# Kernel optimization log

Measured on AMD Instinct MI355X. Metric: run time of the kernel, lower is better.

## Reference

```python
import jax, jax.numpy as jnp
import numpy as np

DIM = 1024
NUM_HEADS = 16
HEAD_DIM = DIM // NUM_HEADS
SCALE = HEAD_DIM ** -0.5


def apply_rope(x):
    # x: [B, H, S, D]; rotate pairs (x1, x2) split as first/second half of D
    S, D = x.shape[-2], x.shape[-1]
    pos = jnp.arange(S, dtype=jnp.float32)[:, None]                      # [S, 1]
    freqs = jnp.exp(jnp.arange(0, D, 2, dtype=jnp.float32) * (-np.log(10000.0) / D))  # [D/2]
    emb = pos * freqs                                                    # [S, D/2]
    cos = jnp.cos(emb)[None, None, :, :].astype(x.dtype)                 # [1,1,S,D/2]
    sin = jnp.sin(emb)[None, None, :, :].astype(x.dtype)
    x1, x2 = jnp.split(x, 2, axis=-1)
    return jnp.concatenate([x1 * cos - x2 * sin, x1 * sin + x2 * cos], axis=-1)


def setup_inputs() -> dict:
    key = jax.random.key(0)
    ks = jax.random.split(key, 6)
    B, S = 2, 2048
    x = jax.random.normal(ks[0], (B, S, DIM), dtype=jnp.float32)
    # torch nn.Linear weights: [out_features, in_features]
    w_std = DIM ** -0.5
    wq = jax.random.normal(ks[1], (DIM, DIM), dtype=jnp.float32) * w_std
    wk = jax.random.normal(ks[2], (DIM, DIM), dtype=jnp.float32) * w_std
    wv = jax.random.normal(ks[3], (DIM, DIM), dtype=jnp.float32) * w_std
    wo = jax.random.normal(ks[4], (DIM, DIM), dtype=jnp.float32) * w_std
    wo_b = jax.random.normal(ks[5], (DIM,), dtype=jnp.float32) * 0.01
    return {"x": x, "wq": wq, "wk": wk, "wv": wv, "wo": wo, "wo_b": wo_b}


def reference(x, wq, wk, wv, wo, wo_b):
    B, S, _ = x.shape
    def proj(w):
        # y = x @ w.T -> [B, S, dim] -> [B, H, S, head_dim]
        y = jnp.einsum('bsd,ed->bse', x, w)
        return y.reshape(B, S, NUM_HEADS, HEAD_DIM).transpose(0, 2, 1, 3)
    q = apply_rope(proj(wq))
    k = apply_rope(proj(wk))
    v = proj(wv)
    attn = jnp.einsum('bhqd,bhkd->bhqk', q, k) * SCALE   # [B,H,S,S]
    attn = jax.nn.softmax(attn, axis=-1)                 # dropout is identity in eval
    out = jnp.einsum('bhqk,bhkd->bhqd', attn, v)         # [B,H,S,D]
    out = out.transpose(0, 2, 1, 3).reshape(B, S, DIM)
    return jnp.einsum('bsd,ed->bse', out, wo) + wo_b
```

## Files before the change

### kernel.cpp

```cpp
#include <hip/hip_runtime.h>
#include <hip/hip_bf16.h>

typedef __attribute__((ext_vector_type(8))) short s16x8;
typedef __attribute__((ext_vector_type(4))) short s16x4;
typedef __attribute__((ext_vector_type(4))) float f32x4;

#define SEQ 2048
#define NB 2
#define NH 16
#define HD 64
#define DIM 1024
#define MR (NB * SEQ)
#define NT (SEQ / 64)
#define QSC 0.18033688011112042f

__device__ __forceinline__ unsigned short f2b(float f) {
    unsigned u = __float_as_uint(f);
    u += 0x7fffu + ((u >> 16) & 1u);
    return (unsigned short)(u >> 16);
}

__device__ __forceinline__ unsigned pk2(float a, float b) {
    unsigned r;
    asm("v_cvt_pk_bf16_f32 %0, %1, %2" : "=v"(r) : "v"(a), "v"(b));
    return r;
}

__device__ __forceinline__ s16x8 mk8(unsigned a, unsigned b, unsigned c, unsigned d) {
    union { unsigned u[4]; s16x8 v; } x;
    x.u[0] = a; x.u[1] = b; x.u[2] = c; x.u[3] = d;
    return x.v;
}

__device__ __forceinline__ s16x8 cat8(s16x4 a, s16x4 b) {
    union { s16x4 h[2]; s16x8 v; } x;
    x.h[0] = a; x.h[1] = b;
    return x.v;
}

__device__ __forceinline__ void gl_lds16(const unsigned short* g, unsigned short* l) {
    __builtin_amdgcn_global_load_lds(
        (const __attribute__((address_space(1))) void*)g,
        (__attribute__((address_space(3))) void*)l, 16, 0, 0);
}

__device__ __forceinline__ unsigned ldsoff(const void* p) {
    return (unsigned)(size_t)(const __attribute__((address_space(3))) void*)p;
}

__device__ __forceinline__ void cast4(const float* __restrict__ src, unsigned short* __restrict__ dst, int i) {
    float4 v = reinterpret_cast<const float4*>(src)[i];
    ushort4 o;
    o.x = f2b(v.x); o.y = f2b(v.y); o.z = f2b(v.z); o.w = f2b(v.w);
    reinterpret_cast<ushort4*>(dst)[i] = o;
}

__global__ __launch_bounds__(256) void prep_kernel(
    const float* __restrict__ x, const float* __restrict__ wq, const float* __restrict__ wk,
    const float* __restrict__ wv, const float* __restrict__ wo,
    unsigned short* __restrict__ xb, unsigned short* __restrict__ wqkv,
    unsigned short* __restrict__ wwo, float2* __restrict__ tab)
{
    int b = blockIdx.x, t = threadIdx.x;
    if (b < 4096)       cast4(x,  xb,                 b * 256 + t);
    else if (b < 5120)  cast4(wq, wqkv,               (b - 4096) * 256 + t);
    else if (b < 6144)  cast4(wk, wqkv + DIM * DIM,   (b - 5120) * 256 + t);
    else if (b < 7168)  cast4(wv, wqkv + 2 * DIM * DIM, (b - 6144) * 256 + t);
    else if (b < 8192)  cast4(wo, wwo,                (b - 7168) * 256 + t);
    else {
        int i = (b - 8192) * 256 + t;
        int pos = i >> 5, fi = i & 31;
        float freq = expf((float)fi * (-9.210340371976184f / 32.0f));
        float emb = (float)pos * freq;
        tab[i] = make_float2(cosf(emb), sinf(emb));
    }
}

template <int EPI>
__global__ __launch_bounds__(256) void gemm_mw(
    const unsigned short* __restrict__ A,
    const unsigned short* __restrict__ Bw,
    const float2* __restrict__ tab,
    unsigned short* __restrict__ qw,
    unsigned short* __restrict__ kw,
    unsigned short* __restrict__ vw,
    float* __restrict__ out,
    const float* __restrict__ bias)
{
    __shared__ unsigned short As[2][4096];
    __shared__ unsigned short Bs[2][4096];
    const int t = threadIdx.x;
    const int wid = t >> 6, lane = t & 63;
    const int wr = wid >> 1, wc = wid & 1;
    const int lo = lane & 15, hi = lane >> 4;
    const int wg = blockIdx.x;
    const int xcd = wg & 7, bi = wg >> 3;
    const int by = xcd * 4 + (bi & 3);
    const int bx = bi >> 2;
    const int m0 = by * 128, n0 = bx * 128;

    const unsigned short* agp = A + (long)(m0 + (t >> 2)) * DIM + (t & 3) * 8;
    const unsigned short* bgp = Bw + (long)(n0 + (t >> 2)) * DIM + (t & 3) * 8;
    unsigned short* alds = &As[0][0] + wid * 512;
    unsigned short* blds = &Bs[0][0] + wid * 512;

#define STG(buf, k0) {                                        \
        gl_lds16(agp + (k0), alds + (buf) * 4096);            \
        gl_lds16(agp + (k0) + 64 * DIM, alds + (buf) * 4096 + 2048); \
        gl_lds16(bgp + (k0), blds + (buf) * 4096);            \
        gl_lds16(bgp + (k0) + 64 * DIM, blds + (buf) * 4096 + 2048); }

    f32x4 acc[4][4] = {};
    STG(0, 0)
    STG(1, 32)

    for (int kt = 0; kt < 32; ++kt) {
        const int cb = kt & 1;
        if (kt < 31) { asm volatile("s_waitcnt vmcnt(4)" ::: "memory"); }
        else         { asm volatile("s_waitcnt vmcnt(0)" ::: "memory"); }
        __builtin_amdgcn_sched_barrier(0);
        __builtin_amdgcn_s_barrier();
        __builtin_amdgcn_sched_barrier(0);
        s16x8 af[4], bf[4];
#pragma unroll
        for (int i = 0; i < 4; ++i)
            af[i] = *reinterpret_cast<const s16x8*>(&As[cb][(wr * 64 + i * 16 + lo) * 32 + hi * 8]);
#pragma unroll
        for (int j = 0; j < 4; ++j)
            bf[j] = *reinterpret_cast<const s16x8*>(&Bs[cb][(wc * 64 + j * 16 + lo) * 32 + hi * 8]);
        asm volatile("s_waitcnt lgkmcnt(0)" ::: "memory");
        __builtin_amdgcn_sched_barrier(0);
        if (kt + 2 < 32) {
            __builtin_amdgcn_s_barrier();
            __builtin_amdgcn_sched_barrier(0);
            STG(cb, (kt + 2) * 32)
        }
        __builtin_amdgcn_s_setprio(1);
#pragma unroll
        for (int i = 0; i < 4; ++i)
#pragma unroll
            for (int j = 0; j < 4; ++j)
                acc[i][j] = __builtin_amdgcn_mfma_f32_16x16x32_bf16(af[i], bf[j], acc[i][j], 0, 0, 0);
        __builtin_amdgcn_s_setprio(0);
    }
#undef STG

    const int rowb = m0 + wr * 64;
    const int colb = n0 + wc * 64;
    if (EPI == 0) {
#pragma unroll
        for (int ai = 0; ai < 4; ++ai) {
#pragma unroll
            for (int cp = 0; cp < 2; ++cp) {
                f32x4 v1 = acc[ai][cp];
                f32x4 v2 = acc[ai][cp + 2];
                int e = colb + cp * 16 + lo;
                int which = e >> 10;
                int eh = e & 1023;
                int h = eh >> 6, d = eh & 63;
                unsigned short* dst = (which == 0) ? qw : ((which == 1) ? kw : vw);
                float qs = (which == 0) ? QSC : 1.0f;
#pragma unroll
                for (int r = 0; r < 4; ++r) {
                    int m = rowb + ai * 16 + hi * 4 + r;
                    int b = m >> 11, pos = m & (SEQ - 1);
                    long off = (((long)(b * NH + h)) * SEQ + pos) * HD;
                    if (which == 2) {
                        dst[off + d]      = f2b(v1[r]);
                        dst[off + d + 32] = f2b(v2[r]);
                    } else {
                        float2 cs = tab[pos * 32 + d];
                        dst[off + d]      = f2b((v1[r] * cs.x - v2[r] * cs.y) * qs);
                        dst[off + d + 32] = f2b((v1[r] * cs.y + v2[r] * cs.x) * qs);
                    }
                }
            }
        }
    } else {
#pragma unroll
        for (int ai = 0; ai < 4; ++ai)
#pragma unroll
            for (int cj = 0; cj < 4; ++cj) {
                int n = colb + cj * 16 + lo;
                float bv = bias[n];
#pragma unroll
                for (int r = 0; r < 4; ++r) {
                    int m = rowb + ai * 16 + hi * 4 + r;
                    out[(long)m * DIM + n] = acc[ai][cj][r] + bv;
                }
            }
    }
}

template <int EPI>
__global__ __launch_bounds__(64, 2) void gemm_async(
    const unsigned short* __restrict__ A,
    const unsigned short* __restrict__ Bw,
    const float2* __restrict__ tab,
    unsigned short* __restrict__ qw,
    unsigned short* __restrict__ kw,
    unsigned short* __restrict__ vw,
    float* __restrict__ out,
    const float* __restrict__ bias)
{
    __shared__ unsigned short As[2 * 2048];
    __shared__ unsigned short Bs[2 * 4096];
    const int lane = threadIdx.x & 63;
    const int lo = lane & 15, hi = lane >> 4;
    const int wg = blockIdx.x;
    const int xcd = wg & 7, bi = wg >> 3;
    const int bx = bi >> 3;
    const int by = xcd * 8 + (bi & 7);
    const int m0 = by * 64, n0 = bx * 128;

    const unsigned short* agp = A + (long)(m0 + (lane >> 2)) * DIM + (lane & 3) * 8;
    const unsigned short* bgp = Bw + (long)(n0 + (lane >> 2)) * DIM + (lane & 3) * 8;

    f32x4 acc[4][8] = {};

#define STG(buf, k0) {                                       \
        unsigned short* al = &As[(buf) * 2048];              \
        unsigned short* bl = &Bs[(buf) * 4096];              \
        _Pragma("unroll") for (int s = 0; s < 4; ++s)        \
            gl_lds16(agp + (k0) + (long)s * 16 * DIM, al + s * 512); \
        _Pragma("unroll") for (int s = 0; s < 8; ++s)        \
            gl_lds16(bgp + (k0) + (long)s * 16 * DIM, bl + s * 512); }

    STG(0, 0)
    STG(1, 32)

    for (int kt = 0; kt < 32; ++kt) {
        const int cb = kt & 1;
        if (kt < 31) { asm volatile("s_waitcnt vmcnt(12)" ::: "memory"); }
        else         { asm volatile("s_waitcnt vmcnt(0)" ::: "memory"); }
        __builtin_amdgcn_sched_barrier(0);
        s16x8 af[4], bf[8];
#pragma unroll
        for (int i = 0; i < 4; ++i)
            af[i] = *reinterpret_cast<const s16x8*>(&As[cb * 2048 + (i * 16 + lo) * 32 + hi * 8]);
#pragma unroll
        for (int j = 0; j < 8; ++j)
            bf[j] = *reinterpret_cast<const s16x8*>(&Bs[cb * 4096 + (j * 16 + lo) * 32 + hi * 8]);
        asm volatile("s_waitcnt lgkmcnt(0)" ::: "memory");
        __builtin_amdgcn_sched_barrier(0);
        if (kt + 2 < 32) STG(cb, (kt + 2) * 32)
        __builtin_amdgcn_sched_barrier(0);
        __builtin_amdgcn_s_setprio(1);
#pragma unroll
        for (int i = 0; i < 4; ++i)
#pragma unroll
            for (int j = 0; j < 8; ++j)
                acc[i][j] = __builtin_amdgcn_mfma_f32_16x16x32_bf16(af[i], bf[j], acc[i][j], 0, 0, 0);
        __builtin_amdgcn_s_setprio(0);
    }
#undef STG

    if (EPI == 0) {
    } else {
#pragma unroll
        for (int ai = 0; ai < 4; ++ai)
#pragma unroll
            for (int bj = 0; bj < 8; ++bj) {
                int n = n0 + bj * 16 + lo;
                float bv = bias[n];
#pragma unroll
                for (int r = 0; r < 4; ++r) {
                    int m = m0 + ai * 16 + hi * 4 + r;
                    out[(long)m * DIM + n] = acc[ai][bj][r] + bv;
                }
            }
    }
}

__global__ __launch_bounds__(256) void flash_attn(
    const unsigned short* __restrict__ qw,
    const unsigned short* __restrict__ kw,
    const unsigned short* __restrict__ vw,
    unsigned short* __restrict__ ao)
{
    __shared__ __align__(16) unsigned char smem[66560];
    const int t = threadIdx.x;
    const int w = t >> 6, lane = t & 63;
    const int lo = lane & 15, hi = lane >> 4;
    const int wg = blockIdx.x;
    const int swz = (wg & 7) * 128 + (wg >> 3);
    const int bh = swz >> 5;
    const int q0 = (swz & 31) * 64;
    const unsigned short* qh = qw + (long)bh * SEQ * HD;
    const unsigned short* kh = kw + (long)bh * SEQ * HD;
    const unsigned short* vh = vw + (long)bh * SEQ * HD;

    s16x8 qf[4][2];
#pragma unroll
    for (int qt = 0; qt < 4; ++qt)
#pragma unroll
        for (int ds = 0; ds < 2; ++ds)
            qf[qt][ds] = *reinterpret_cast<const s16x8*>(
                qh + (long)(q0 + qt * 16 + lo) * HD + ds * 32 + hi * 8);
    asm volatile("s_waitcnt vmcnt(0)" ::: "memory");

    unsigned char* wbase = smem + w * 16384;
    const int kr0 = lane >> 3, ks0 = (lane & 7) ^ (kr0 & 7);
    const int kr1 = 8 + (lane >> 3), ks1 = (lane & 7) ^ (kr1 & 7);
    const unsigned short* ksrc0 = kh + (16 * w + kr0) * HD + ks0 * 8;
    const unsigned short* ksrc1 = kh + (16 * w + kr1) * HD + ks1 * 8;
    const int c0 = lane, c1 = 64 + lane;
    const int kl0 = ((c0 >> 3 >> 2) << 2) | ((c0 >> 1) & 3);
    const int dd0 = (((c0 >> 3) & 3) << 4) | ((c0 & 1) << 3);
    const int kl1 = ((c1 >> 3 >> 2) << 2) | ((c1 >> 1) & 3);
    const int dd1 = (((c1 >> 3) & 3) << 4) | ((c1 & 1) << 3);
    const unsigned short* vsrc0 = vh + (16 * w + kl0) * HD + dd0;
    const unsigned short* vsrc1 = vh + (16 * w + kl1) * HD + dd1;

#define STAGE(buf, kb) {                                              \
        unsigned short* d_ = (unsigned short*)(wbase + (buf) * 4096); \
        gl_lds16(ksrc0 + (kb) * HD, d_);                              \
        gl_lds16(ksrc1 + (kb) * HD, d_ + 512);                        \
        gl_lds16(vsrc0 + (kb) * HD, d_ + 1024);                       \
        gl_lds16(vsrc1 + (kb) * HD, d_ + 1536); }

    const int kro0 = lo * 128 + ((hi ^ (lo & 7)) << 4);
    const int kro1 = lo * 128 + (((4 + hi) ^ (lo & 7)) << 4);
    const unsigned vtb0 = ldsoff(wbase) + 2048 + hi * 512 + lo * 8;

    f32x4 od[4][4] = {};
    f32x4 lr = {0.f, 0.f, 0.f, 0.f};

    STAGE(0, 0)
    STAGE(1, 64)
    STAGE(2, 128)
    STAGE(3, 192)

    constexpr int NT2 = NT / 2;
    for (int i2 = 0; i2 < NT2; ++i2) {
        const int b0 = (2 * i2) & 3;
        if (i2 < NT2 - 1) { asm volatile("s_waitcnt vmcnt(8)" ::: "memory"); }
        else              { asm volatile("s_waitcnt vmcnt(0)" ::: "memory"); }
        __builtin_amdgcn_sched_barrier(0);

        const unsigned char* bp0 = wbase + b0 * 4096;
        const unsigned char* bp1 = bp0 + 4096;
        s16x8 kf0 = *reinterpret_cast<const s16x8*>(bp0 + kro0);
        s16x8 kf1 = *reinterpret_cast<const s16x8*>(bp0 + kro1);
        s16x8 kg0 = *reinterpret_cast<const s16x8*>(bp1 + kro0);
        s16x8 kg1 = *reinterpret_cast<const s16x8*>(bp1 + kro1);
        const unsigned vta = vtb0 + b0 * 4096;
        const unsigned vtb = vta + 4096;
        s16x4 va0, va1, va2, va3, vb0, vb1, vb2, vb3;
        asm volatile("ds_read_b64_tr_b16 %0, %1"            : "=v"(va0) : "v"(vta));
        asm volatile("ds_read_b64_tr_b16 %0, %1 offset:128" : "=v"(va1) : "v"(vta));
        asm volatile("ds_read_b64_tr_b16 %0, %1 offset:256" : "=v"(va2) : "v"(vta));
        asm volatile("ds_read_b64_tr_b16 %0, %1 offset:384" : "=v"(va3) : "v"(vta));
        asm volatile("ds_read_b64_tr_b16 %0, %1"            : "=v"(vb0) : "v"(vtb));
        asm volatile("ds_read_b64_tr_b16 %0, %1 offset:128" : "=v"(vb1) : "v"(vtb));
        asm volatile("ds_read_b64_tr_b16 %0, %1 offset:256" : "=v"(vb2) : "v"(vtb));
        asm volatile("ds_read_b64_tr_b16 %0, %1 offset:384" : "=v"(vb3) : "v"(vtb));
        asm volatile("s_waitcnt lgkmcnt(0)" ::: "memory");
        __builtin_amdgcn_sched_barrier(0);

        if (i2 < NT2 - 2) {
            STAGE(b0, (2 * i2 + 4) * 64)
            STAGE(b0 + 1, (2 * i2 + 5) * 64)
        }
        __builtin_amdgcn_sched_barrier(0);

        f32x4 sc[4] = {}, sd[4] = {};
        __builtin_amdgcn_s_setprio(1);
#pragma unroll
        for (int qt = 0; qt < 4; ++qt) {
            sc[qt] = __builtin_amdgcn_mfma_f32_16x16x32_bf16(kf0, qf[qt][0], sc[qt], 0, 0, 0);
            sd[qt] = __builtin_amdgcn_mfma_f32_16x16x32_bf16(kg0, qf[qt][0], sd[qt], 0, 0, 0);
        }
#pragma unroll
        for (int qt = 0; qt < 4; ++qt) {
            sc[qt] = __builtin_amdgcn_mfma_f32_16x16x32_bf16(kf1, qf[qt][1], sc[qt], 0, 0, 0);
            sd[qt] = __builtin_amdgcn_mfma_f32_16x16x32_bf16(kg1, qf[qt][1], sd[qt], 0, 0, 0);
        }
        __builtin_amdgcn_s_setprio(0);

        s16x8 pf8[4];
#pragma unroll
        for (int qt = 0; qt < 4; ++qt) {
            float a0 = exp2f(sc[qt][0]), a1 = exp2f(sc[qt][1]);
            float a2 = exp2f(sc[qt][2]), a3 = exp2f(sc[qt][3]);
            float b0e = exp2f(sd[qt][0]), b1e = exp2f(sd[qt][1]);
            float b2e = exp2f(sd[qt][2]), b3e = exp2f(sd[qt][3]);
            lr[qt] += ((a0 + a1) + (a2 + a3)) + ((b0e + b1e) + (b2e + b3e));
            pf8[qt] = mk8(pk2(a0, a1), pk2(a2, a3), pk2(b0e, b1e), pk2(b2e, b3e));
        }
        s16x8 vf80 = cat8(va0, vb0), vf81 = cat8(va1, vb1);
        s16x8 vf82 = cat8(va2, vb2), vf83 = cat8(va3, vb3);

        __builtin_amdgcn_s_setprio(1);
#pragma unroll
        for (int qt = 0; qt < 4; ++qt) {
            od[0][qt] = __builtin_amdgcn_mfma_f32_16x16x32_bf16(vf80, pf8[qt], od[0][qt], 0, 0, 0);
            od[1][qt] = __builtin_amdgcn_mfma_f32_16x16x32_bf16(vf81, pf8[qt], od[1][qt], 0, 0, 0);
            od[2][qt] = __builtin_amdgcn_mfma_f32_16x16x32_bf16(vf82, pf8[qt], od[2][qt], 0, 0, 0);
            od[3][qt] = __builtin_amdgcn_mfma_f32_16x16x32_bf16(vf83, pf8[qt], od[3][qt], 0, 0, 0);
        }
        __builtin_amdgcn_s_setprio(0);
    }
#undef STAGE

#pragma unroll
    for (int qt = 0; qt < 4; ++qt) {
        lr[qt] += __shfl_xor(lr[qt], 16);
        lr[qt] += __shfl_xor(lr[qt], 32);
    }
    float* red = reinterpret_cast<float*>(smem);
    float* ldl = reinterpret_cast<float*>(smem + 65536);
    if (lane < 16) {
#pragma unroll
        for (int qt = 0; qt < 4; ++qt) ldl[w * 64 + qt * 16 + lane] = lr[qt];
    }

    const int b = bh >> 4, h = bh & 15;
    const int ql = w * 16 + (lane >> 2);
    const int qc = ql & 7;
    float linv = 0.f;
#pragma unroll
    for (int p = 0; p < 2; ++p) {
        __syncthreads();
#pragma unroll
        for (int dtp = 0; dtp < 2; ++dtp) {
#pragma unroll
            for (int qt = 0; qt < 4; ++qt) {
                int q = qt * 16 + lo;
                int quad = ((dtp << 2) + hi) ^ (lo & 7);
                *reinterpret_cast<f32x4*>(red + w * 4096 + q * 32 + quad * 4) = od[p * 2 + dtp][qt];
            }
        }
        __syncthreads();
        float s0[8] = {0.f, 0.f, 0.f, 0.f, 0.f, 0.f, 0.f, 0.f};
#pragma unroll
        for (int w2 = 0; w2 < 4; ++w2)
#pragma unroll
            for (int k = 0; k < 2; ++k) {
                int quad = (((lane & 3) << 1) + k) ^ qc;
                f32x4 v = *reinterpret_cast<const f32x4*>(red + w2 * 4096 + ql * 32 + quad * 4);
#pragma unroll
                for (int j = 0; j < 4; ++j) s0[k * 4 + j] += v[j];
            }
        if (p == 0)
            linv = 1.f / (ldl[ql] + ldl[64 + ql] + ldl[128 + ql] + ldl[192 + ql]);
        unsigned uu[4];
#pragma unroll
        for (int k2 = 0; k2 < 4; ++k2)
            uu[k2] = pk2(s0[2 * k2] * linv, s0[2 * k2 + 1] * linv);
        int4 ov;
        ov.x = uu[0]; ov.y = uu[1]; ov.z = uu[2]; ov.w = uu[3];
        *reinterpret_cast<int4*>(ao + ((long)(b * SEQ + q0 + ql)) * DIM +
                                 h * 64 + p * 32 + (lane & 3) * 8) = ov;
    }
}

extern "C" void kernel_launch(void* const* d_in, const int* in_sizes, int n_in,
                              void* d_out, int out_size, void* d_ws, size_t ws_size,
                              hipStream_t stream) {
    const float* x   = (const float*)d_in[0];
    const float* wq  = (const float*)d_in[1];
    const float* wk  = (const float*)d_in[2];
    const float* wv  = (const float*)d_in[3];
    const float* wo  = (const float*)d_in[4];
    const float* wob = (const float*)d_in[5];

    char* ws = (char*)d_ws;
    unsigned short* xb   = (unsigned short*)(ws);
    unsigned short* wqkv = (unsigned short*)(ws + 8388608);
    unsigned short* wwo  = (unsigned short*)(ws + 14680064);
    unsigned short* qw   = (unsigned short*)(ws + 16777216);
    unsigned short* kw   = (unsigned short*)(ws + 25165824);
    unsigned short* vw   = (unsigned short*)(ws + 33554432);
    unsigned short* ao   = (unsigned short*)(ws + 41943040);
    float2* tab          = (float2*)(ws + 50331648);

    prep_kernel<<<8448, 256, 0, stream>>>(x, wq, wk, wv, wo, xb, wqkv, wwo, tab);

    gemm_mw<0><<<768, 256, 0, stream>>>(xb, wqkv, tab, qw, kw, vw, nullptr, nullptr);
    flash_attn<<<1024, 256, 0, stream>>>(qw, kw, vw, ao);
    gemm_async<1><<<512, 64, 0, stream>>>(ao, wwo, nullptr, nullptr, nullptr, nullptr,
                                          (float*)d_out, wob);
}
```

Measured before the change: 129.9 us.

## Split attention queries across waves with shared K/V tiles instead of key split

Restructures the flash attention kernel so each wave handles 16 query rows while all waves share cooperatively staged, double-buffered K/V tiles. This eliminates the end-of-kernel cross-wave reduction through shared memory and halves the LDS footprint, which may raise occupancy. In exchange it adds block-wide barriers per key tile and increases LDS fragment reads per MFMA, since each K/V fragment now serves fewer queries.

```diff
diff --git a/kernel.cpp b/kernel.cpp
--- a/kernel.cpp
+++ b/kernel.cpp
@@ -255,8 +255,7 @@
     }
 #undef STG
 
-    if (EPI == 0) {
-    } else {
+    if (EPI == 1) {
 #pragma unroll
         for (int ai = 0; ai < 4; ++ai)
 #pragma unroll
@@ -278,7 +277,7 @@
     const unsigned short* __restrict__ vw,
     unsigned short* __restrict__ ao)
 {
-    __shared__ __align__(16) unsigned char smem[66560];
+    __shared__ __align__(16) unsigned char smem[32768];
     const int t = threadIdx.x;
     const int w = t >> 6, lane = t & 63;
     const int lo = lane & 15, hi = lane >> 4;
@@ -290,168 +289,125 @@
     const unsigned short* kh = kw + (long)bh * SEQ * HD;
     const unsigned short* vh = vw + (long)bh * SEQ * HD;
 
-    s16x8 qf[4][2];
-#pragma unroll
-    for (int qt = 0; qt < 4; ++qt)
-#pragma unroll
-        for (int ds = 0; ds < 2; ++ds)
-            qf[qt][ds] = *reinterpret_cast<const s16x8*>(
-                qh + (long)(q0 + qt * 16 + lo) * HD + ds * 32 + hi * 8);
+    s16x8 qf[2];
+#pragma unroll
+    for (int ds = 0; ds < 2; ++ds)
+        qf[ds] = *reinterpret_cast<const s16x8*>(
+            qh + (long)(q0 + w * 16 + lo) * HD + ds * 32 + hi * 8);
     asm volatile("s_waitcnt vmcnt(0)" ::: "memory");
 
-    unsigned char* wbase = smem + w * 16384;
-    const int kr0 = lane >> 3, ks0 = (lane & 7) ^ (kr0 & 7);
-    const int kr1 = 8 + (lane >> 3), ks1 = (lane & 7) ^ (kr1 & 7);
-    const unsigned short* ksrc0 = kh + (16 * w + kr0) * HD + ks0 * 8;
-    const unsigned short* ksrc1 = kh + (16 * w + kr1) * HD + ks1 * 8;
-    const int c0 = lane, c1 = 64 + lane;
-    const int kl0 = ((c0 >> 3 >> 2) << 2) | ((c0 >> 1) & 3);
-    const int dd0 = (((c0 >> 3) & 3) << 4) | ((c0 & 1) << 3);
-    const int kl1 = ((c1 >> 3 >> 2) << 2) | ((c1 >> 1) & 3);
-    const int dd1 = (((c1 >> 3) & 3) << 4) | ((c1 & 1) << 3);
-    const unsigned short* vsrc0 = vh + (16 * w + kl0) * HD + dd0;
-    const unsigned short* vsrc1 = vh + (16 * w + kl1) * HD + dd1;
-
-#define STAGE(buf, kb) {                                              \
-        unsigned short* d_ = (unsigned short*)(wbase + (buf) * 4096); \
-        gl_lds16(ksrc0 + (kb) * HD, d_);                              \
-        gl_lds16(ksrc1 + (kb) * HD, d_ + 512);                        \
-        gl_lds16(vsrc0 + (kb) * HD, d_ + 1024);                       \
-        gl_lds16(vsrc1 + (kb) * HD, d_ + 1536); }
-
-    const int kro0 = lo * 128 + ((hi ^ (lo & 7)) << 4);
-    const int kro1 = lo * 128 + (((4 + hi) ^ (lo & 7)) << 4);
-    const unsigned vtb0 = ldsoff(wbase) + 2048 + hi * 512 + lo * 8;
-
-    f32x4 od[4][4] = {};
-    f32x4 lr = {0.f, 0.f, 0.f, 0.f};
+    const int kc0 = w * 64 + lane, kc1 = 256 + kc0;
+    const int krow0 = kc0 >> 3, kslot0 = (kc0 & 7) ^ (krow0 & 7);
+    const int krow1 = kc1 >> 3, kslot1 = (kc1 & 7) ^ (krow1 & 7);
+    const unsigned short* ksrc0 = kh + (long)krow0 * HD + kslot0 * 8;
+    const unsigned short* ksrc1 = kh + (long)krow1 * HD + kslot1 * 8;
+    const int vk0 = ((kc0 >> 5) << 2) | ((kc0 & 7) >> 1);
+    const int vd0 = ((kc0 >> 3) & 3) * 16 + (kc0 & 1) * 8;
+    const int vk1 = ((kc1 >> 5) << 2) | ((kc1 & 7) >> 1);
+    const int vd1 = ((kc1 >> 3) & 3) * 16 + (kc1 & 1) * 8;
+    const unsigned short* vsrc0 = vh + (long)vk0 * HD + vd0;
+    const unsigned short* vsrc1 = vh + (long)vk1 * HD + vd1;
+
+    unsigned short* kd0 = (unsigned short*)(smem) + w * 512;
+    unsigned short* kd1 = (unsigned short*)(smem) + 2048 + w * 512;
+    unsigned short* vd0p = (unsigned short*)(smem) + 4096 + w * 512;
+    unsigned short* vd1p = (unsigned short*)(smem) + 6144 + w * 512;
+
+#define STAGE(buf, kb) {                                   \
+        gl_lds16(ksrc0 + (long)(kb) * HD, kd0 + (buf) * 8192); \
+        gl_lds16(ksrc1 + (long)(kb) * HD, kd1 + (buf) * 8192); \
+        gl_lds16(vsrc0 + (long)(kb) * HD, vd0p + (buf) * 8192); \
+        gl_lds16(vsrc1 + (long)(kb) * HD, vd1p + (buf) * 8192); }
+
+    const int kroA = lo * 128 + ((hi ^ (lo & 7)) << 4);
+    const int kroB = lo * 128 + (((4 + hi) ^ (lo & 7)) << 4);
+    const unsigned vtb0 = ldsoff(smem) + 8192 + hi * 512 + lo * 8;
+
+    f32x4 od[4] = {};
+    float lr = 0.f;
 
     STAGE(0, 0)
     STAGE(1, 64)
-    STAGE(2, 128)
-    STAGE(3, 192)
-
-    constexpr int NT2 = NT / 2;
-    for (int i2 = 0; i2 < NT2; ++i2) {
-        const int b0 = (2 * i2) & 3;
-        if (i2 < NT2 - 1) { asm volatile("s_waitcnt vmcnt(8)" ::: "memory"); }
-        else              { asm volatile("s_waitcnt vmcnt(0)" ::: "memory"); }
-        __builtin_amdgcn_sched_barrier(0);
-
-        const unsigned char* bp0 = wbase + b0 * 4096;
-        const unsigned char* bp1 = bp0 + 4096;
-        s16x8 kf0 = *reinterpret_cast<const s16x8*>(bp0 + kro0);
-        s16x8 kf1 = *reinterpret_cast<const s16x8*>(bp0 + kro1);
-        s16x8 kg0 = *reinterpret_cast<const s16x8*>(bp1 + kro0);
-        s16x8 kg1 = *reinterpret_cast<const s16x8*>(bp1 + kro1);
-        const unsigned vta = vtb0 + b0 * 4096;
-        const unsigned vtb = vta + 4096;
-        s16x4 va0, va1, va2, va3, vb0, vb1, vb2, vb3;
-        asm volatile("ds_read_b64_tr_b16 %0, %1"            : "=v"(va0) : "v"(vta));
-        asm volatile("ds_read_b64_tr_b16 %0, %1 offset:128" : "=v"(va1) : "v"(vta));
-        asm volatile("ds_read_b64_tr_b16 %0, %1 offset:256" : "=v"(va2) : "v"(vta));
-        asm volatile("ds_read_b64_tr_b16 %0, %1 offset:384" : "=v"(va3) : "v"(vta));
-        asm volatile("ds_read_b64_tr_b16 %0, %1"            : "=v"(vb0) : "v"(vtb));
-        asm volatile("ds_read_b64_tr_b16 %0, %1 offset:128" : "=v"(vb1) : "v"(vtb));
-        asm volatile("ds_read_b64_tr_b16 %0, %1 offset:256" : "=v"(vb2) : "v"(vtb));
-        asm volatile("ds_read_b64_tr_b16 %0, %1 offset:384" : "=v"(vb3) : "v"(vtb));
+
+    for (int kt = 0; kt < NT; ++kt) {
+        const int cb = kt & 1;
+        if (kt < NT - 1) { asm volatile("s_waitcnt vmcnt(4)" ::: "memory"); }
+        else             { asm volatile("s_waitcnt vmcnt(0)" ::: "memory"); }
+        __builtin_amdgcn_sched_barrier(0);
+        __builtin_amdgcn_s_barrier();
+        __builtin_amdgcn_sched_barrier(0);
+
+        const unsigned char* bp = smem + cb * 16384;
+        s16x8 kf[4][2];
+#pragma unroll
+        for (int cj = 0; cj < 4; ++cj) {
+            kf[cj][0] = *reinterpret_cast<const s16x8*>(bp + cj * 2048 + kroA);
+            kf[cj][1] = *reinterpret_cast<const s16x8*>(bp + cj * 2048 + kroB);
+        }
+        s16x4 vt[2][2][4];
+#pragma unroll
+        for (int kk = 0; kk < 2; ++kk)
+#pragma unroll
+            for (int half = 0; half < 2; ++half) {
+                const unsigned vb = vtb0 + cb * 16384 + kk * 4096 + half * 2048;
+                asm volatile("ds_read_b64_tr_b16 %0, %1"            : "=v"(vt[kk][half][0]) : "v"(vb));
+                asm volatile("ds_read_b64_tr_b16 %0, %1 offset:128" : "=v"(vt[kk][half][1]) : "v"(vb));
+                asm volatile("ds_read_b64_tr_b16 %0, %1 offset:256" : "=v"(vt[kk][half][2]) : "v"(vb));
+                asm volatile("ds_read_b64_tr_b16 %0, %1 offset:384" : "=v"(vt[kk][half][3]) : "v"(vb));
+            }
         asm volatile("s_waitcnt lgkmcnt(0)" ::: "memory");
         __builtin_amdgcn_sched_barrier(0);
-
-        if (i2 < NT2 - 2) {
-            STAGE(b0, (2 * i2 + 4) * 64)
-            STAGE(b0 + 1, (2 * i2 + 5) * 64)
-        }
-        __builtin_amdgcn_sched_barrier(0);
-
-        f32x4 sc[4] = {}, sd[4] = {};
+        if (kt + 2 < NT) {
+            __builtin_amdgcn_s_barrier();
+            __builtin_amdgcn_sched_barrier(0);
+            STAGE(cb, (kt + 2) * 64)
+        }
+
+        f32x4 sc[4] = {};
         __builtin_amdgcn_s_setprio(1);
 #pragma unroll
-        for (int qt = 0; qt < 4; ++qt) {
-            sc[qt] = __builtin_amdgcn_mfma_f32_16x16x32_bf16(kf0, qf[qt][0], sc[qt], 0, 0, 0);
-            sd[qt] = __builtin_amdgcn_mfma_f32_16x16x32_bf16(kg0, qf[qt][0], sd[qt], 0, 0, 0);
-        }
-#pragma unroll
-        for (int qt = 0; qt < 4; ++qt) {
-            sc[qt] = __builtin_amdgcn_mfma_f32_16x16x32_bf16(kf1, qf[qt][1], sc[qt], 0, 0, 0);
-            sd[qt] = __builtin_amdgcn_mfma_f32_16x16x32_bf16(kg1, qf[qt][1], sd[qt], 0, 0, 0);
-        }
+        for (int cj = 0; cj < 4; ++cj)
+            sc[cj] = __builtin_amdgcn_mfma_f32_16x16x32_bf16(kf[cj][0], qf[0], sc[cj], 0, 0, 0);
+#pragma unroll
+        for (int cj = 0; cj < 4; ++cj)
+            sc[cj] = __builtin_amdgcn_mfma_f32_16x16x32_bf16(kf[cj][1], qf[1], sc[cj], 0, 0, 0);
         __builtin_amdgcn_s_setprio(0);
 
-        s16x8 pf8[4];
-#pragma unroll
-        for (int qt = 0; qt < 4; ++qt) {
-            float a0 = exp2f(sc[qt][0]), a1 = exp2f(sc[qt][1]);
-            float a2 = exp2f(sc[qt][2]), a3 = exp2f(sc[qt][3]);
-            float b0e = exp2f(sd[qt][0]), b1e = exp2f(sd[qt][1]);
-            float b2e = exp2f(sd[qt][2]), b3e = exp2f(sd[qt][3]);
-            lr[qt] += ((a0 + a1) + (a2 + a3)) + ((b0e + b1e) + (b2e + b3e));
-            pf8[qt] = mk8(pk2(a0, a1), pk2(a2, a3), pk2(b0e, b1e), pk2(b2e, b3e));
-        }
-        s16x8 vf80 = cat8(va0, vb0), vf81 = cat8(va1, vb1);
-        s16x8 vf82 = cat8(va2, vb2), vf83 = cat8(va3, vb3);
+        s16x8 pf8[2];
+#pragma unroll
+        for (int kk = 0; kk < 2; ++kk) {
+            float a0 = exp2f(sc[2 * kk][0]), a1 = exp2f(sc[2 * kk][1]);
+            float a2 = exp2f(sc[2 * kk][2]), a3 = exp2f(sc[2 * kk][3]);
+            float b0 = exp2f(sc[2 * kk + 1][0]), b1 = exp2f(sc[2 * kk + 1][1]);
+            float b2 = exp2f(sc[2 * kk + 1][2]), b3 = exp2f(sc[2 * kk + 1][3]);
+            lr += ((a0 + a1) + (a2 + a3)) + ((b0 + b1) + (b2 + b3));
+            pf8[kk] = mk8(pk2(a0, a1), pk2(a2, a3), pk2(b0, b1), pk2(b2, b3));
+        }
 
         __builtin_amdgcn_s_setprio(1);
 #pragma unroll
-        for (int qt = 0; qt < 4; ++qt) {
-            od[0][qt] = __builtin_amdgcn_mfma_f32_16x16x32_bf16(vf80, pf8[qt], od[0][qt], 0, 0, 0);
-            od[1][qt] = __builtin_amdgcn_mfma_f32_16x16x32_bf16(vf81, pf8[qt], od[1][qt], 0, 0, 0);
-            od[2][qt] = __builtin_amdgcn_mfma_f32_16x16x32_bf16(vf82, pf8[qt], od[2][qt], 0, 0, 0);
-            od[3][qt] = __builtin_amdgcn_mfma_f32_16x16x32_bf16(vf83, pf8[qt], od[3][qt], 0, 0, 0);
+        for (int kk = 0; kk < 2; ++kk) {
+#pragma unroll
+            for (int dt = 0; dt < 4; ++dt) {
+                s16x8 vf8 = cat8(vt[kk][0][dt], vt[kk][1][dt]);
+                od[dt] = __builtin_amdgcn_mfma_f32_16x16x32_bf16(vf8, pf8[kk], od[dt], 0, 0, 0);
+            }
         }
         __builtin_amdgcn_s_setprio(0);
     }
 #undef STAGE
 
-#pragma unroll
-    for (int qt = 0; qt < 4; ++qt) {
-        lr[qt] += __shfl_xor(lr[qt], 16);
-        lr[qt] += __shfl_xor(lr[qt], 32);
-    }
-    float* red = reinterpret_cast<float*>(smem);
-    float* ldl = reinterpret_cast<float*>(smem + 65536);
-    if (lane < 16) {
-#pragma unroll
-        for (int qt = 0; qt < 4; ++qt) ldl[w * 64 + qt * 16 + lane] = lr[qt];
-    }
-
+    lr += __shfl_xor(lr, 16);
+    lr += __shfl_xor(lr, 32);
+    float linv = 1.f / lr;
     const int b = bh >> 4, h = bh & 15;
-    const int ql = w * 16 + (lane >> 2);
-    const int qc = ql & 7;
-    float linv = 0.f;
-#pragma unroll
-    for (int p = 0; p < 2; ++p) {
-        __syncthreads();
-#pragma unroll
-        for (int dtp = 0; dtp < 2; ++dtp) {
-#pragma unroll
-            for (int qt = 0; qt < 4; ++qt) {
-                int q = qt * 16 + lo;
-                int quad = ((dtp << 2) + hi) ^ (lo & 7);
-                *reinterpret_cast<f32x4*>(red + w * 4096 + q * 32 + quad * 4) = od[p * 2 + dtp][qt];
-            }
-        }
-        __syncthreads();
-        float s0[8] = {0.f, 0.f, 0.f, 0.f, 0.f, 0.f, 0.f, 0.f};
-#pragma unroll
-        for (int w2 = 0; w2 < 4; ++w2)
-#pragma unroll
-            for (int k = 0; k < 2; ++k) {
-                int quad = (((lane & 3) << 1) + k) ^ qc;
-                f32x4 v = *reinterpret_cast<const f32x4*>(red + w2 * 4096 + ql * 32 + quad * 4);
-#pragma unroll
-                for (int j = 0; j < 4; ++j) s0[k * 4 + j] += v[j];
-            }
-        if (p == 0)
-            linv = 1.f / (ldl[ql] + ldl[64 + ql] + ldl[128 + ql] + ldl[192 + ql]);
-        unsigned uu[4];
-#pragma unroll
-        for (int k2 = 0; k2 < 4; ++k2)
-            uu[k2] = pk2(s0[2 * k2] * linv, s0[2 * k2 + 1] * linv);
-        int4 ov;
-        ov.x = uu[0]; ov.y = uu[1]; ov.z = uu[2]; ov.w = uu[3];
-        *reinterpret_cast<int4*>(ao + ((long)(b * SEQ + q0 + ql)) * DIM +
-                                 h * 64 + p * 32 + (lane & 3) * 8) = ov;
+    const int qg = q0 + w * 16 + lo;
+#pragma unroll
+    for (int dt = 0; dt < 4; ++dt) {
+        uint2 u;
+        u.x = pk2(od[dt][0] * linv, od[dt][1] * linv);
+        u.y = pk2(od[dt][2] * linv, od[dt][3] * linv);
+        *reinterpret_cast<uint2*>(ao + ((long)(b * SEQ + qg)) * DIM + h * 64 + dt * 16 + hi * 4) = u;
     }
 }
 
```

Result: slower. 135.6 us (+4.4%).
